# Performance work log

Hardware: AMD Instinct MI355X
Metric: run time of the kernel (lower is better)

## Reference

```python
import jax, jax.numpy as jnp
import numpy as np

B, N, S, K, D = 8, 16384, 1024, 32, 64
MLP = [64, 64, 128]
C_IN = 3 + D  # grouped_xyz_norm (3) concat grouped point features (D)
EPS = 1e-5


def setup_inputs() -> dict:
    key = jax.random.key(0)
    ks = jax.random.split(key, 16)
    inp = {
        "xyz": jax.random.normal(ks[0], (B, 3, N), dtype=jnp.float32),
        "points": jax.random.normal(ks[1], (B, D, N), dtype=jnp.float32),
        "sample_idx": jax.random.randint(ks[2], (B, S), 0, N, dtype=jnp.int32),
    }
    last = C_IN
    for i, oc in enumerate(MLP):
        scale = 1.0 / np.sqrt(last)
        inp[f"w{i}"] = jax.random.uniform(ks[3 + 4 * i], (oc, last), jnp.float32, -scale, scale)
        inp[f"b{i}"] = jax.random.uniform(ks[4 + 4 * i], (oc,), jnp.float32, -scale, scale)
        inp[f"g{i}"] = jnp.ones((oc,), jnp.float32)   # BN gamma
        inp[f"be{i}"] = jnp.zeros((oc,), jnp.float32)  # BN beta
        last = oc
    return inp


def _gather(pts, idx):
    # pts: [B,N,C], idx: [B,...] -> [B,...,C]
    return jax.vmap(lambda p, i: p[i])(pts, idx)


def _mlp_layer(x, w, b, g, be):
    # x: [B,C,K,S]; 1x1 Conv2d + BatchNorm2d (training-mode batch stats) + ReLU
    y = jnp.einsum("bcks,oc->boks", x, w) + b[None, :, None, None]
    mu = jnp.mean(y, axis=(0, 2, 3), keepdims=True)
    var = jnp.var(y, axis=(0, 2, 3), keepdims=True)
    y = (y - mu) * jax.lax.rsqrt(var + EPS)
    y = y * g[None, :, None, None] + be[None, :, None, None]
    return jax.nn.relu(y)


def reference(xyz, points, sample_idx, w0, b0, g0, be0, w1, b1, g1, be1, w2, b2, g2, be2):
    xyz_t = jnp.transpose(xyz, (0, 2, 1))      # [B,N,3]
    pts_t = jnp.transpose(points, (0, 2, 1))   # [B,N,D]
    idx_s = sample_idx.astype(jnp.int32)

    new_xyz = _gather(xyz_t, idx_s)            # [B,S,3]

    # square_distance(new_xyz, xyz): [B,S,N]
    d = (jnp.sum(new_xyz ** 2, -1)[:, :, None]
         + jnp.sum(xyz_t ** 2, -1)[:, None, :]
         - 2.0 * jnp.einsum("bsc,bnc->bsn", new_xyz, xyz_t))
    _, idx = jax.lax.top_k(-d, K)              # kNN indices [B,S,K]

    grouped_xyz = _gather(xyz_t, idx)          # [B,S,K,3]
    grouped_norm = grouped_xyz - new_xyz[:, :, None, :]
    grouped_pts = _gather(pts_t, idx)          # [B,S,K,D]
    feat = jnp.concatenate([grouped_norm, grouped_pts], axis=-1)  # [B,S,K,3+D]

    x = jnp.transpose(feat, (0, 3, 2, 1))      # [B,C,K,S]
    x = _mlp_layer(x, w0, b0, g0, be0)
    x = _mlp_layer(x, w1, b1, g1, be1)
    x = _mlp_layer(x, w2, b2, g2, be2)
    new_points = jnp.max(x, axis=2)            # [B,128,S]

    return (jnp.transpose(new_xyz, (0, 2, 1)), new_points, grouped_xyz, idx_s)
```

## Files before the change

### kernel.cpp

```cpp
#include <hip/hip_runtime.h>

constexpr int cB = 8, cN = 16384, cS = 1024, cK = 32, cD = 64;
constexpr int cO2 = 128;
constexpr int PTOT = cB * cS * cK;
constexpr int NBLK = PTOT / 64;
constexpr int C2POS = 128;
constexpr int NBLK2 = PTOT / C2POS;

constexpr int OUT1_OFF = cB * 3 * cS;
constexpr int OUT2_OFF = OUT1_OFF + cB * cO2 * cS;
constexpr int OUT3_OFF = OUT2_OFF + cB * cS * cK * 3;

constexpr size_t WS_PTS  = 0;
constexpr size_t WS_XYZP = WS_PTS  + (size_t)cB * cN * cD * 4;
constexpr size_t WS_IDX  = WS_XYZP + (size_t)cB * cN * 16;
constexpr size_t WS_NORM = WS_IDX  + (size_t)PTOT * 4;
constexpr size_t WS_Y0   = WS_NORM + (size_t)PTOT * 3 * 4;
constexpr size_t WS_Y1   = WS_Y0   + (size_t)PTOT * 64 * 4;
constexpr size_t WS_MX   = WS_Y1   + (size_t)PTOT * 64 * 4;
constexpr size_t WS_MN   = WS_MX   + (size_t)cB * cS * cO2 * 4;
constexpr size_t WS_P0   = WS_MN   + (size_t)cB * cS * cO2 * 4;
constexpr size_t WS_P1   = WS_P0   + (size_t)NBLK * 64 * 2 * 8;
constexpr size_t WS_P2   = WS_P1   + (size_t)NBLK * 64 * 2 * 8;
constexpr size_t WS_BN   = WS_P2   + (size_t)NBLK * 128 * 2 * 8;
constexpr size_t WS_END  = WS_BN   + 3 * 128 * 2 * 4;

__device__ __forceinline__ unsigned keyOf(float d) {
    unsigned u = __float_as_uint(d);
    return u ^ ((unsigned)((int)u >> 31) | 0x80000000u);
}
__device__ __forceinline__ float distNp(float qx, float qy, float qz, float sq, float4 p) {
    float m0 = __fmul_rn(qx, p.x);
    float m1 = __fmul_rn(qy, p.y);
    float m2 = __fmul_rn(qz, p.z);
    float dt = __fadd_rn(__fadd_rn(m0, m1), m2);
    return __fsub_rn(__fadd_rn(sq, p.w), __fmul_rn(2.0f, dt));
}

__global__ __launch_bounds__(256) void k_pack(const float* __restrict__ xyz,
                                              float4* __restrict__ xyzp) {
    int i = blockIdx.x * 256 + threadIdx.x;
    int b = i >> 14, n = i & (cN - 1);
    float x = xyz[(b * 3 + 0) * cN + n];
    float y = xyz[(b * 3 + 1) * cN + n];
    float z = xyz[(b * 3 + 2) * cN + n];
    float sq = __fadd_rn(__fadd_rn(__fmul_rn(x, x), __fmul_rn(y, y)), __fmul_rn(z, z));
    xyzp[i] = make_float4(x, y, z, sq);
}

__global__ __launch_bounds__(256) void k_tr(const float* __restrict__ pts,
                                            float* __restrict__ ptsT) {
    __shared__ float tile[64][65];
    int b = blockIdx.y;
    int n0 = blockIdx.x * 64;
    int tid = threadIdx.x;
    for (int it = 0; it < 16; ++it) {
        int l = it * 256 + tid;
        int c = l >> 6, nn = l & 63;
        tile[nn][c] = pts[((size_t)b * 64 + c) * cN + n0 + nn];
    }
    __syncthreads();
    for (int it = 0; it < 16; ++it) {
        int l = it * 256 + tid;
        int nn = l >> 6, c = l & 63;
        ptsT[((size_t)(b * cN + n0 + nn)) * 64 + c] = tile[nn][c];
    }
}

#define QB 8
#define CAP 256

__device__ __forceinline__ void selectBin2(const unsigned* __restrict__ h, int lane,
                                           int target, int* Tout, int* cbOut) {
    int base = lane * 8;
    unsigned hh[8];
    unsigned c8 = 0;
#pragma unroll
    for (int i = 0; i < 8; i++) { hh[i] = h[base + i]; c8 += hh[i]; }
    unsigned incl = c8;
#pragma unroll
    for (int off = 1; off < 32; off <<= 1) {
        unsigned t = __shfl_up(incl, (unsigned)off, 32);
        if (lane >= off) incl += t;
    }
    int excl = (int)(incl - c8);
    if (excl < target && target <= (int)incl) {
        int c = excl;
#pragma unroll
        for (int i = 0; i < 8; i++) {
            int nc = c + (int)hh[i];
            if (c < target && target <= nc) { *Tout = base + i; *cbOut = c; }
            c = nc;
        }
    }
}

__global__ __launch_bounds__(256, 4) void k_knn(const float* __restrict__ xyz,
                                                const int* __restrict__ sidx_g,
                                                const float4* __restrict__ xyzp,
                                                int* __restrict__ idxw,
                                                float* __restrict__ normw,
                                                float* __restrict__ outbuf) {
    __shared__ unsigned hist[QB][258];
    __shared__ unsigned long long cand[QB][CAP];
    __shared__ unsigned cnt[QB];
    __shared__ float qxs[QB], qys[QB], qzs[QB], sqs[QB];
    __shared__ int sIdx[QB];
    __shared__ float s1s[QB], tAs[QB], tBs[QB];
    __shared__ int T1s[QB], cb1s[QB], T2s[QB], cb2s[QB];
    __shared__ float tAcc[QB];
    __shared__ int refq[QB];
    __shared__ int anyRef;
    __shared__ unsigned order[QB][cK];

    int tid = threadIdx.x;
    int qi = tid >> 5, lane = tid & 31;
    int qbase = blockIdx.x * QB;
    int b = qbase / cS;
    int s0 = qbase % cS;
    const float4* pb = xyzp + (size_t)b * cN;

    if (tid < QB) {
        int si = sidx_g[b * cS + s0 + tid];
        sIdx[tid] = si;
        float x = xyz[(b * 3 + 0) * cN + si];
        float y = xyz[(b * 3 + 1) * cN + si];
        float z = xyz[(b * 3 + 2) * cN + si];
        qxs[tid] = x; qys[tid] = y; qzs[tid] = z;
        sqs[tid] = __fadd_rn(__fadd_rn(__fmul_rn(x, x), __fmul_rn(y, y)), __fmul_rn(z, z));
        cnt[tid] = 0u;
    }
    if (tid == 0) anyRef = 0;
    for (int i = tid; i < QB * 258; i += 256) ((unsigned*)hist)[i] = 0u;
    __syncthreads();

    {
        float qx = qxs[qi], qy = qys[qi], qz = qzs[qi], qsq = sqs[qi];
        float dmin = 3.4e38f;
        for (int t = 0; t < 64; ++t) {
            float4 p = pb[lane + 32 * t];
            float dot = fmaf(qx, p.x, fmaf(qy, p.y, qz * p.z));
            float d = fmaf(-2.0f, dot, qsq + p.w);
            dmin = fminf(dmin, d);
        }
        float rmax = dmin;
#pragma unroll
        for (int off = 16; off; off >>= 1)
            rmax = fmaxf(rmax, __shfl_xor(rmax, off, 32));
        if (lane == 0) {
            float R = fmaxf(rmax, 1e-12f);
            float s1 = 254.0f / R;
            s1s[qi] = s1;
            tAs[qi] = qsq * s1;
            tBs[qi] = -2.0f * s1;
        }
    }
    __syncthreads();

    float lqx[QB], lqy[QB], lqz[QB], lS[QB], lA[QB], lB[QB];
#pragma unroll
    for (int q = 0; q < QB; q++) {
        lqx[q] = qxs[q]; lqy[q] = qys[q]; lqz[q] = qzs[q];
        lS[q] = s1s[q]; lA[q] = tAs[q]; lB[q] = tBs[q];
    }

    for (int j = 0; j < cN / 256; ++j) {
        float4 p = pb[j * 256 + tid];
#pragma unroll
        for (int q = 0; q < QB; ++q) {
            float dot = fmaf(lqx[q], p.x, fmaf(lqy[q], p.y, lqz[q] * p.z));
            float t = fmaf(dot, lB[q], fmaf(p.w, lS[q], lA[q]));
            if (t < 258.0f) {
                int bin = __float2int_rz(fmaxf(t, 0.0f));
                atomicAdd(&hist[q][bin], 1u);
            }
        }
    }
    __syncthreads();

    selectBin2(hist[qi], lane, cK, &T1s[qi], &cb1s[qi]);
    __syncthreads();
    if (tid < QB) {
        int T1 = T1s[tid];
        int acc = cb1s[tid] + (int)hist[tid][T1] + (int)hist[tid][T1 + 1];
        int nr = (acc > CAP) ? 1 : 0;
        refq[tid] = nr;
        tAcc[tid] = (float)(T1 + 2);
        if (nr) atomicOr(&anyRef, 1);
    }
    __syncthreads();

    if (anyRef) {
        for (int i = tid; i < QB * 258; i += 256) ((unsigned*)hist)[i] = 0u;
        __syncthreads();
        int lT1[QB], lrf[QB];
#pragma unroll
        for (int q = 0; q < QB; q++) { lT1[q] = T1s[q]; lrf[q] = refq[q]; }
        for (int j = 0; j < cN / 256; ++j) {
            float4 p = pb[j * 256 + tid];
#pragma unroll
            for (int q = 0; q < QB; ++q) {
                if (lrf[q]) {
                    float dot = fmaf(lqx[q], p.x, fmaf(lqy[q], p.y, lqz[q] * p.z));
                    float t = fmaf(dot, lB[q], fmaf(p.w, lS[q], lA[q]));
                    float um = fmaxf(t, 0.0f) - (float)lT1[q];
                    if (um >= 0.0f && um < 2.0f) {
                        int sub = min(255, __float2int_rz(um * 128.0f));
                        atomicAdd(&hist[q][sub], 1u);
                    }
                }
            }
        }
        __syncthreads();
        if (refq[qi]) selectBin2(hist[qi], lane, cK - cb1s[qi], &T2s[qi], &cb2s[qi]);
        __syncthreads();
        if (tid < QB && refq[tid])
            tAcc[tid] = (float)T1s[tid] + (float)(T2s[tid] + 2) * 0.0078125f;
        __syncthreads();
    }

    float lsq[QB], lt[QB];
#pragma unroll
    for (int q = 0; q < QB; q++) { lsq[q] = sqs[q]; lt[q] = tAcc[q]; }

    for (int j = 0; j < cN / 256; ++j) {
        int n = j * 256 + tid;
        float4 p = pb[n];
#pragma unroll
        for (int q = 0; q < QB; ++q) {
            float dot = fmaf(lqx[q], p.x, fmaf(lqy[q], p.y, lqz[q] * p.z));
            float t = fmaf(dot, lB[q], fmaf(p.w, lS[q], lA[q]));
            if (t < lt[q]) {
                float de = distNp(lqx[q], lqy[q], lqz[q], lsq[q], p);
                unsigned pos = atomicAdd(&cnt[q], 1u);
                if (pos < CAP)
                    cand[q][pos] = ((unsigned long long)keyOf(de) << 32) | (unsigned)n;
            }
        }
    }
    __syncthreads();

    int m = (int)min(cnt[qi], (unsigned)CAP);
    for (int r = 0; r < cK; ++r) {
        unsigned long long best = ~0ull;
        int bslot = -1;
        for (int i = lane; i < m; i += 32) {
            unsigned long long v = cand[qi][i];
            if (v < best) { best = v; bslot = i; }
        }
#pragma unroll
        for (int off = 16; off; off >>= 1) {
            unsigned long long ov = __shfl_xor(best, off, 32);
            int os = __shfl_xor(bslot, off, 32);
            if (ov < best) { best = ov; bslot = os; }
        }
        if (lane == 0) {
            order[qi][r] = (best != ~0ull) ? (unsigned)(best & 0xFFFFFFFFull) : 0u;
            if (bslot >= 0) cand[qi][bslot] = ~0ull;
        }
    }

    {
        int r = lane;
        int s = s0 + qi;
        int n = (int)order[qi][r];
        size_t pos = (size_t)(b * cS + s) * cK + r;
        idxw[pos] = n;
        float px = xyz[(b * 3 + 0) * cN + n];
        float py = xyz[(b * 3 + 1) * cN + n];
        float pz = xyz[(b * 3 + 2) * cN + n];
        outbuf[OUT2_OFF + pos * 3 + 0] = px;
        outbuf[OUT2_OFF + pos * 3 + 1] = py;
        outbuf[OUT2_OFF + pos * 3 + 2] = pz;
        normw[pos * 3 + 0] = __fsub_rn(px, qxs[qi]);
        normw[pos * 3 + 1] = __fsub_rn(py, qys[qi]);
        normw[pos * 3 + 2] = __fsub_rn(pz, qzs[qi]);
        if (r == 0) {
            outbuf[OUT3_OFF + b * cS + s] = (float)sIdx[qi];
            outbuf[(b * 3 + 0) * cS + s] = qxs[qi];
            outbuf[(b * 3 + 1) * cS + s] = qys[qi];
            outbuf[(b * 3 + 2) * cS + s] = qzs[qi];
        }
    }
}

__global__ __launch_bounds__(256) void k_conv0(const int* __restrict__ idxw,
                                               const float* __restrict__ normw,
                                               const float* __restrict__ ptsT,
                                               const float* __restrict__ w0,
                                               const float* __restrict__ b0,
                                               float* __restrict__ y0,
                                               double* __restrict__ part0) {
    __shared__ __align__(16) float fA[64][68];
    __shared__ __align__(16) float wT[68 * 68];
    __shared__ float ps[16][64];
    __shared__ float pq[16][64];
    __shared__ float bl[64];
    int tid = threadIdx.x;
    int blk = blockIdx.x;
    int b = blk >> 9;
    int s0 = (blk & 511) << 1;
    size_t posbase = ((size_t)b * cS + s0) * cK;

    for (int l = tid; l < 64 * 67; l += 256) {
        int o = l / 67, c = l - o * 67;
        wT[c * 68 + o] = w0[l];
    }
    if (tid < 68) wT[67 * 68 + tid] = 0.0f;
    if (tid < 64) bl[tid] = b0[tid];
    {
        int kk = tid >> 2, p = tid & 3;
        size_t pos = posbase + kk;
        int n = idxw[pos];
        const float* pr = ptsT + ((size_t)b * cN + n) * 64 + p * 16;
        float* frow = &fA[kk][3 + p * 16];
#pragma unroll
        for (int q4 = 0; q4 < 4; q4++) {
            float4 v = *(const float4*)(pr + q4 * 4);
            frow[q4 * 4 + 0] = v.x; frow[q4 * 4 + 1] = v.y;
            frow[q4 * 4 + 2] = v.z; frow[q4 * 4 + 3] = v.w;
        }
        if (p == 0) {
            fA[kk][0] = normw[pos * 3 + 0];
            fA[kk][1] = normw[pos * 3 + 1];
            fA[kk][2] = normw[pos * 3 + 2];
            fA[kk][67] = 0.0f;
        }
    }
    __syncthreads();

    int ty = tid >> 4, tx = tid & 15;
    float acc[4][4];
#pragma unroll
    for (int i = 0; i < 4; i++)
#pragma unroll
        for (int j = 0; j < 4; j++) acc[i][j] = bl[tx * 4 + j];

    for (int c4 = 0; c4 < 17; ++c4) {
        float4 wv[4];
#pragma unroll
        for (int cc = 0; cc < 4; cc++)
            wv[cc] = *(const float4*)&wT[(c4 * 4 + cc) * 68 + tx * 4];
#pragma unroll
        for (int i = 0; i < 4; i++) {
            float4 a = *(const float4*)&fA[ty * 4 + i][c4 * 4];
            acc[i][0] = fmaf(a.x, wv[0].x, acc[i][0]);
            acc[i][1] = fmaf(a.x, wv[0].y, acc[i][1]);
            acc[i][2] = fmaf(a.x, wv[0].z, acc[i][2]);
            acc[i][3] = fmaf(a.x, wv[0].w, acc[i][3]);
            acc[i][0] = fmaf(a.y, wv[1].x, acc[i][0]);
            acc[i][1] = fmaf(a.y, wv[1].y, acc[i][1]);
            acc[i][2] = fmaf(a.y, wv[1].z, acc[i][2]);
            acc[i][3] = fmaf(a.y, wv[1].w, acc[i][3]);
            acc[i][0] = fmaf(a.z, wv[2].x, acc[i][0]);
            acc[i][1] = fmaf(a.z, wv[2].y, acc[i][1]);
            acc[i][2] = fmaf(a.z, wv[2].z, acc[i][2]);
            acc[i][3] = fmaf(a.z, wv[2].w, acc[i][3]);
            acc[i][0] = fmaf(a.w, wv[3].x, acc[i][0]);
            acc[i][1] = fmaf(a.w, wv[3].y, acc[i][1]);
            acc[i][2] = fmaf(a.w, wv[3].z, acc[i][2]);
            acc[i][3] = fmaf(a.w, wv[3].w, acc[i][3]);
        }
    }
#pragma unroll
    for (int i = 0; i < 4; i++) {
        int kk = ty * 4 + i;
        float4 o4 = make_float4(acc[i][0], acc[i][1], acc[i][2], acc[i][3]);
        *(float4*)(y0 + (posbase + kk) * 64 + tx * 4) = o4;
    }
#pragma unroll
    for (int j = 0; j < 4; j++) {
        float s = acc[0][j] + acc[1][j] + acc[2][j] + acc[3][j];
        float q = acc[0][j] * acc[0][j] + acc[1][j] * acc[1][j] +
                  acc[2][j] * acc[2][j] + acc[3][j] * acc[3][j];
        ps[ty][tx * 4 + j] = s;
        pq[ty][tx * 4 + j] = q;
    }
    __syncthreads();
    if (tid < 64) {
        float s = 0.f, q = 0.f;
        for (int t = 0; t < 16; t++) { s += ps[t][tid]; q += pq[t][tid]; }
        part0[((size_t)blk * 64 + tid) * 2 + 0] = (double)s;
        part0[((size_t)blk * 64 + tid) * 2 + 1] = (double)q;
    }
}

__global__ __launch_bounds__(256) void k_conv1(const float* __restrict__ yin,
                                               const float2* __restrict__ bnin,
                                               const float* __restrict__ w,
                                               const float* __restrict__ bb,
                                               float* __restrict__ yout,
                                               double* __restrict__ part) {
    __shared__ __align__(16) float fA[64][68];
    __shared__ __align__(16) float wT[64 * 68];
    __shared__ float ps[16][64];
    __shared__ float pq[16][64];
    __shared__ float bl[64], al[64], sl[64];
    int tid = threadIdx.x;
    int blk = blockIdx.x;
    int b = blk >> 9;
    int s0 = (blk & 511) << 1;
    size_t posbase = ((size_t)b * cS + s0) * cK;

    if (tid < 64) {
        bl[tid] = bb[tid];
        float2 t = bnin[tid];
        al[tid] = t.x; sl[tid] = t.y;
    }
    __syncthreads();
    for (int l = tid; l < 64 * 64; l += 256) {
        int o = l >> 6, c = l & 63;
        wT[c * 68 + o] = w[l];
    }
    {
        int kk = tid >> 2, p = tid & 3;
        const float* yr = yin + (posbase + kk) * 64 + p * 16;
#pragma unroll
        for (int q4 = 0; q4 < 4; q4++) {
            float4 v = *(const float4*)(yr + q4 * 4);
            int c = p * 16 + q4 * 4;
            v.x = fmaxf(fmaf(v.x, al[c + 0], sl[c + 0]), 0.0f);
            v.y = fmaxf(fmaf(v.y, al[c + 1], sl[c + 1]), 0.0f);
            v.z = fmaxf(fmaf(v.z, al[c + 2], sl[c + 2]), 0.0f);
            v.w = fmaxf(fmaf(v.w, al[c + 3], sl[c + 3]), 0.0f);
            *(float4*)&fA[kk][c] = v;
        }
    }
    __syncthreads();

    int ty = tid >> 4, tx = tid & 15;
    float acc[4][4];
#pragma unroll
    for (int i = 0; i < 4; i++)
#pragma unroll
        for (int j = 0; j < 4; j++) acc[i][j] = bl[tx * 4 + j];

    for (int c4 = 0; c4 < 16; ++c4) {
        float4 wv[4];
#pragma unroll
        for (int cc = 0; cc < 4; cc++)
            wv[cc] = *(const float4*)&wT[(c4 * 4 + cc) * 68 + tx * 4];
#pragma unroll
        for (int i = 0; i < 4; i++) {
            float4 a = *(const float4*)&fA[ty * 4 + i][c4 * 4];
            acc[i][0] = fmaf(a.x, wv[0].x, acc[i][0]);
            acc[i][1] = fmaf(a.x, wv[0].y, acc[i][1]);
            acc[i][2] = fmaf(a.x, wv[0].z, acc[i][2]);
            acc[i][3] = fmaf(a.x, wv[0].w, acc[i][3]);
            acc[i][0] = fmaf(a.y, wv[1].x, acc[i][0]);
            acc[i][1] = fmaf(a.y, wv[1].y, acc[i][1]);
            acc[i][2] = fmaf(a.y, wv[1].z, acc[i][2]);
            acc[i][3] = fmaf(a.y, wv[1].w, acc[i][3]);
            acc[i][0] = fmaf(a.z, wv[2].x, acc[i][0]);
            acc[i][1] = fmaf(a.z, wv[2].y, acc[i][1]);
            acc[i][2] = fmaf(a.z, wv[2].z, acc[i][2]);
            acc[i][3] = fmaf(a.z, wv[2].w, acc[i][3]);
            acc[i][0] = fmaf(a.w, wv[3].x, acc[i][0]);
            acc[i][1] = fmaf(a.w, wv[3].y, acc[i][1]);
            acc[i][2] = fmaf(a.w, wv[3].z, acc[i][2]);
            acc[i][3] = fmaf(a.w, wv[3].w, acc[i][3]);
        }
    }
#pragma unroll
    for (int i = 0; i < 4; i++) {
        int kk = ty * 4 + i;
        float4 o4 = make_float4(acc[i][0], acc[i][1], acc[i][2], acc[i][3]);
        *(float4*)(yout + (posbase + kk) * 64 + tx * 4) = o4;
    }
#pragma unroll
    for (int j = 0; j < 4; j++) {
        float s = acc[0][j] + acc[1][j] + acc[2][j] + acc[3][j];
        float q = acc[0][j] * acc[0][j] + acc[1][j] * acc[1][j] +
                  acc[2][j] * acc[2][j] + acc[3][j] * acc[3][j];
        ps[ty][tx * 4 + j] = s;
        pq[ty][tx * 4 + j] = q;
    }
    __syncthreads();
    if (tid < 64) {
        float s = 0.f, q = 0.f;
        for (int t = 0; t < 16; t++) { s += ps[t][tid]; q += pq[t][tid]; }
        part[((size_t)blk * 64 + tid) * 2 + 0] = (double)s;
        part[((size_t)blk * 64 + tid) * 2 + 1] = (double)q;
    }
}

__global__ __launch_bounds__(256) void k_conv2(const float* __restrict__ y1,
                                               const float2* __restrict__ bn1,
                                               const float* __restrict__ w2,
                                               const float* __restrict__ b2,
                                               float* __restrict__ mx,
                                               float* __restrict__ mn,
                                               double* __restrict__ part2) {
    __shared__ __align__(16) float fAT[64 * 132];
    __shared__ __align__(16) float wT[64 * 132];
    __shared__ float al[64], sl[64], bl[128];
    int tid = threadIdx.x;
    int blk = blockIdx.x;
    int b = blk >> 8;
    int s0 = (blk & 255) << 2;
    size_t posbase = ((size_t)b * cS + s0) * cK;

    if (tid < 64) { float2 t = bn1[tid]; al[tid] = t.x; sl[tid] = t.y; }
    if (tid < 128) bl[tid] = b2[tid];
    __syncthreads();

    {
        int r = tid >> 1, half = tid & 1;
        const float* yr = y1 + (posbase + r) * 64 + half * 32;
#pragma unroll
        for (int q = 0; q < 8; q++) {
            float4 v = *(const float4*)(yr + q * 4);
            int c = half * 32 + q * 4;
            v.x = fmaxf(fmaf(v.x, al[c + 0], sl[c + 0]), 0.0f);
            v.y = fmaxf(fmaf(v.y, al[c + 1], sl[c + 1]), 0.0f);
            v.z = fmaxf(fmaf(v.z, al[c + 2], sl[c + 2]), 0.0f);
            v.w = fmaxf(fmaf(v.w, al[c + 3], sl[c + 3]), 0.0f);
            fAT[(c + 0) * 132 + r] = v.x;
            fAT[(c + 1) * 132 + r] = v.y;
            fAT[(c + 2) * 132 + r] = v.z;
            fAT[(c + 3) * 132 + r] = v.w;
        }
    }
    for (int l = tid; l < 128 * 64; l += 256) {
        int o = l >> 6, c = l & 63;
        wT[c * 132 + o] = w2[l];
    }
    __syncthreads();

    int ry = tid >> 4, tx = tid & 15;
    float acc[8][8];
#pragma unroll
    for (int i = 0; i < 8; i++) {
#pragma unroll
        for (int j = 0; j < 4; j++) acc[i][j] = bl[tx * 4 + j];
#pragma unroll
        for (int j = 4; j < 8; j++) acc[i][j] = bl[64 + tx * 4 + (j - 4)];
    }

    for (int c = 0; c < 64; ++c) {
        const float* fb = fAT + c * 132;
        const float* wb = wT + c * 132;
        float4 a0 = *(const float4*)(fb + ry * 8);
        float4 a1 = *(const float4*)(fb + ry * 8 + 4);
        float4 w0v = *(const float4*)(wb + tx * 4);
        float4 w1v = *(const float4*)(wb + 64 + tx * 4);
        float av[8] = {a0.x, a0.y, a0.z, a0.w, a1.x, a1.y, a1.z, a1.w};
        float wv[8] = {w0v.x, w0v.y, w0v.z, w0v.w, w1v.x, w1v.y, w1v.z, w1v.w};
#pragma unroll
        for (int i = 0; i < 8; i++)
#pragma unroll
            for (int j = 0; j < 8; j++)
                acc[i][j] = fmaf(av[i], wv[j], acc[i][j]);
    }
    __syncthreads();

    float* ps  = wT;
    float* pq  = wT + 16 * 128;
    float* pmx = wT + 32 * 128;
    float* pmn = wT + 48 * 128;
#pragma unroll
    for (int j = 0; j < 8; j++) {
        int o = (j < 4) ? (tx * 4 + j) : (64 + tx * 4 + (j - 4));
        float s = 0.f, q = 0.f;
        float mv = -3.402823466e+38f, nv = 3.402823466e+38f;
#pragma unroll
        for (int i = 0; i < 8; i++) {
            float v = acc[i][j];
            s += v; q += v * v;
            mv = fmaxf(mv, v); nv = fminf(nv, v);
        }
        ps[ry * 128 + o] = s;
        pq[ry * 128 + o] = q;
        pmx[ry * 128 + o] = mv;
        pmn[ry * 128 + o] = nv;
    }
    __syncthreads();
    if (tid < 128) {
        float s = 0.f, q = 0.f;
        for (int t = 0; t < 16; t++) { s += ps[t * 128 + tid]; q += pq[t * 128 + tid]; }
        part2[((size_t)blk * 128 + tid) * 2 + 0] = (double)s;
        part2[((size_t)blk * 128 + tid) * 2 + 1] = (double)q;
    }
    for (int e = tid; e < 512; e += 256) {
        int sg = e >> 7, o = e & 127;
        float mv = -3.402823466e+38f, nv = 3.402823466e+38f;
        for (int t = sg * 4; t < sg * 4 + 4; ++t) {
            mv = fmaxf(mv, pmx[t * 128 + o]);
            nv = fminf(nv, pmn[t * 128 + o]);
        }
        int s = s0 + sg;
        mx[((size_t)b * cS + s) * 128 + o] = mv;
        mn[((size_t)b * cS + s) * 128 + o] = nv;
    }
}

__global__ __launch_bounds__(256) void k_fin(const double* __restrict__ part, int nblk,
                                             int oc,
                                             const float* __restrict__ g,
                                             const float* __restrict__ be,
                                             float2* __restrict__ bnout) {
    __shared__ double rs[256], rq[256];
    int o = blockIdx.x;
    int tid = threadIdx.x;
    double s = 0.0, q = 0.0;
    for (int i = tid; i < nblk; i += 256) {
        const double* p = part + ((size_t)i * oc + o) * 2;
        s += p[0];
        q += p[1];
    }
    rs[tid] = s; rq[tid] = q;
    __syncthreads();
    for (int off = 128; off; off >>= 1) {
        if (tid < off) { rs[tid] += rs[tid + off]; rq[tid] += rq[tid + off]; }
        __syncthreads();
    }
    if (tid == 0) {
        double cntv = (double)PTOT;
        double mu = rs[0] / cntv;
        double var = rq[0] / cntv - mu * mu;
        if (var < 0.0) var = 0.0;
        float a = (float)((double)g[o] / sqrt(var + 1e-5));
        float sh = (float)((double)be[o] - mu * (double)a);
        bnout[o] = make_float2(a, sh);
    }
}

__global__ __launch_bounds__(256) void k_final(const float* __restrict__ mx,
                                               const float* __restrict__ mn,
                                               const float2* __restrict__ bn2,
                                               float* __restrict__ out1) {
    int i = blockIdx.x * 256 + threadIdx.x;
    int b = i >> 17;
    int r = i & ((1 << 17) - 1);
    int o = r >> 10;
    int s = r & 1023;
    float2 t = bn2[o];
    size_t idx = ((size_t)b * cS + s) * 128 + o;
    float M = (t.x >= 0.0f) ? mx[idx] : mn[idx];
    out1[i] = fmaxf(t.x * M + t.y, 0.0f);
}

extern "C" void kernel_launch(void* const* d_in, const int* in_sizes, int n_in,
                              void* d_out, int out_size, void* d_ws, size_t ws_size,
                              hipStream_t stream) {
    (void)in_sizes; (void)n_in; (void)out_size;
    const float* xyz = (const float*)d_in[0];
    const float* pts = (const float*)d_in[1];
    const int* sidx  = (const int*)d_in[2];
    const float* w0  = (const float*)d_in[3];
    const float* b0  = (const float*)d_in[4];
    const float* g0  = (const float*)d_in[5];
    const float* be0 = (const float*)d_in[6];
    const float* w1  = (const float*)d_in[7];
    const float* b1  = (const float*)d_in[8];
    const float* g1  = (const float*)d_in[9];
    const float* be1 = (const float*)d_in[10];
    const float* w2  = (const float*)d_in[11];
    const float* b2  = (const float*)d_in[12];
    const float* g2  = (const float*)d_in[13];
    const float* be2 = (const float*)d_in[14];
    float* out = (float*)d_out;
    char* ws = (char*)d_ws;
    if (ws_size < WS_END) return;

    float* ptsT  = (float*)(ws + WS_PTS);
    float4* xyzp = (float4*)(ws + WS_XYZP);
    int* idxw    = (int*)(ws + WS_IDX);
    float* normw = (float*)(ws + WS_NORM);
    float* y0    = (float*)(ws + WS_Y0);
    float* y1    = (float*)(ws + WS_Y1);
    float* mx    = (float*)(ws + WS_MX);
    float* mn    = (float*)(ws + WS_MN);
    double* p0   = (double*)(ws + WS_P0);
    double* p1   = (double*)(ws + WS_P1);
    double* p2   = (double*)(ws + WS_P2);
    float2* bnb  = (float2*)(ws + WS_BN);

    hipLaunchKernelGGL(k_pack, dim3(cB * cN / 256), dim3(256), 0, stream, xyz, xyzp);
    hipLaunchKernelGGL(k_tr, dim3(cN / 64, cB), dim3(256), 0, stream, pts, ptsT);
    hipLaunchKernelGGL(k_knn, dim3(cB * cS / QB), dim3(256), 0, stream,
                       xyz, sidx, xyzp, idxw, normw, out);
    hipLaunchKernelGGL(k_conv0, dim3(NBLK), dim3(256), 0, stream,
                       idxw, normw, ptsT, w0, b0, y0, p0);
    hipLaunchKernelGGL(k_fin, dim3(64), dim3(256), 0, stream, p0, NBLK, 64, g0, be0, bnb);
    hipLaunchKernelGGL(k_conv1, dim3(NBLK), dim3(256), 0, stream, y0, bnb, w1, b1, y1, p1);
    hipLaunchKernelGGL(k_fin, dim3(64), dim3(256), 0, stream, p1, NBLK, 64, g1, be1, bnb + 128);
    hipLaunchKernelGGL(k_conv2, dim3(NBLK2), dim3(256), 0, stream,
                       y1, bnb + 128, w2, b2, mx, mn, p2);
    hipLaunchKernelGGL(k_fin, dim3(128), dim3(256), 0, stream, p2, NBLK2, 128, g2, be2, bnb + 256);
    hipLaunchKernelGGL(k_final, dim3(cB * cO2 * cS / 256), dim3(256), 0, stream,
                       mx, mn, bnb + 256, out + OUT1_OFF);
}
```

Before: 397.4 us.

## Add uniform grid spatial index to restrict kNN scans to nearby cells

Measured after the change: 755.0 us. 90.0% more time.

```diff
diff --git a/kernel.cpp b/kernel.cpp
--- a/kernel.cpp
+++ b/kernel.cpp
@@ -6,6 +6,11 @@
 constexpr int NBLK = PTOT / 64;
 constexpr int C2POS = 128;
 constexpr int NBLK2 = PTOT / C2POS;
+
+constexpr int GR = 32;
+constexpr int GC = GR * GR * GR;
+#define GL 4.5f
+#define GINV (32.0f / 9.0f)
 
 constexpr int OUT1_OFF = cB * 3 * cS;
 constexpr int OUT2_OFF = OUT1_OFF + cB * cO2 * cS;
@@ -25,6 +30,11 @@
 constexpr size_t WS_BN   = WS_P2   + (size_t)NBLK * 128 * 2 * 8;
 constexpr size_t WS_END  = WS_BN   + 3 * 128 * 2 * 4;
 
+constexpr size_t WS_SPT  = WS_Y0;
+constexpr size_t WS_SIX  = WS_SPT + (size_t)cB * cN * 16;
+constexpr size_t WS_CNT  = WS_SIX + (size_t)cB * cN * 4;
+constexpr size_t WS_CST  = WS_CNT + (size_t)cB * GC * 4;
+
 __device__ __forceinline__ unsigned keyOf(float d) {
     unsigned u = __float_as_uint(d);
     return u ^ ((unsigned)((int)u >> 31) | 0x80000000u);
@@ -35,6 +45,13 @@
     float m2 = __fmul_rn(qz, p.z);
     float dt = __fadd_rn(__fadd_rn(m0, m1), m2);
     return __fsub_rn(__fadd_rn(sq, p.w), __fmul_rn(2.0f, dt));
+}
+
+__device__ __forceinline__ int cellClamp(float v) {
+    return min(GR - 1, max(0, (int)floorf((v + GL) * GINV)));
+}
+__device__ __forceinline__ int cellOf(float4 p) {
+    return (cellClamp(p.z) * GR + cellClamp(p.y)) * GR + cellClamp(p.x);
 }
 
 __global__ __launch_bounds__(256) void k_pack(const float* __restrict__ xyz,
@@ -48,23 +65,54 @@
     xyzp[i] = make_float4(x, y, z, sq);
 }
 
-__global__ __launch_bounds__(256) void k_tr(const float* __restrict__ pts,
-                                            float* __restrict__ ptsT) {
-    __shared__ float tile[64][65];
-    int b = blockIdx.y;
-    int n0 = blockIdx.x * 64;
-    int tid = threadIdx.x;
-    for (int it = 0; it < 16; ++it) {
-        int l = it * 256 + tid;
-        int c = l >> 6, nn = l & 63;
-        tile[nn][c] = pts[((size_t)b * 64 + c) * cN + n0 + nn];
-    }
-    __syncthreads();
-    for (int it = 0; it < 16; ++it) {
-        int l = it * 256 + tid;
-        int nn = l >> 6, c = l & 63;
-        ptsT[((size_t)(b * cN + n0 + nn)) * 64 + c] = tile[nn][c];
-    }
+__global__ __launch_bounds__(256) void k_gzero(int* __restrict__ cnt) {
+    int i = blockIdx.x * 256 + threadIdx.x;
+    if (i < cB * GC) cnt[i] = 0;
+}
+
+__global__ __launch_bounds__(256) void k_gcnt(const float4* __restrict__ xyzp,
+                                              int* __restrict__ cnt) {
+    int i = blockIdx.x * 256 + threadIdx.x;
+    int b = i >> 14;
+    atomicAdd(&cnt[b * GC + cellOf(xyzp[i])], 1);
+}
+
+__global__ __launch_bounds__(256) void k_gscan(int* __restrict__ cnt,
+                                               int* __restrict__ cst) {
+    __shared__ int s[256];
+    int b = blockIdx.x, tid = threadIdx.x;
+    const int CB = GC / 256;
+    int base = b * GC + tid * CB;
+    int sum = 0;
+    for (int k = 0; k < CB; ++k) sum += cnt[base + k];
+    s[tid] = sum;
+    __syncthreads();
+    for (int off = 1; off < 256; off <<= 1) {
+        int v = (tid >= off) ? s[tid - off] : 0;
+        __syncthreads();
+        s[tid] += v;
+        __syncthreads();
+    }
+    int run = s[tid] - sum;
+    for (int k = 0; k < CB; ++k) {
+        int v = cnt[base + k];
+        cst[(size_t)b * (GC + 1) + tid * CB + k] = run;
+        cnt[base + k] = run;
+        run += v;
+    }
+    if (tid == 255) cst[(size_t)b * (GC + 1) + GC] = run;
+}
+
+__global__ __launch_bounds__(256) void k_gscat(const float4* __restrict__ xyzp,
+                                               int* __restrict__ cnt,
+                                               float4* __restrict__ spt,
+                                               int* __restrict__ six) {
+    int i = blockIdx.x * 256 + threadIdx.x;
+    int b = i >> 14, n = i & (cN - 1);
+    float4 p = xyzp[i];
+    int pos = atomicAdd(&cnt[b * GC + cellOf(p)], 1);
+    spt[(size_t)b * cN + pos] = p;
+    six[(size_t)b * cN + pos] = n;
 }
 
 #define QB 8
@@ -98,6 +146,9 @@
 __global__ __launch_bounds__(256, 4) void k_knn(const float* __restrict__ xyz,
                                                 const int* __restrict__ sidx_g,
                                                 const float4* __restrict__ xyzp,
+                                                const float4* __restrict__ spt,
+                                                const int* __restrict__ six,
+                                                const int* __restrict__ cellStart,
                                                 int* __restrict__ idxw,
                                                 float* __restrict__ normw,
                                                 float* __restrict__ outbuf) {
@@ -106,7 +157,6 @@
     __shared__ unsigned cnt[QB];
     __shared__ float qxs[QB], qys[QB], qzs[QB], sqs[QB];
     __shared__ int sIdx[QB];
-    __shared__ float s1s[QB], tAs[QB], tBs[QB];
     __shared__ int T1s[QB], cb1s[QB], T2s[QB], cb2s[QB];
     __shared__ float tAcc[QB];
     __shared__ int refq[QB];
@@ -119,6 +169,9 @@
     int b = qbase / cS;
     int s0 = qbase % cS;
     const float4* pb = xyzp + (size_t)b * cN;
+    const float4* sp = spt + (size_t)b * cN;
+    const int* sx = six + (size_t)b * cN;
+    const int* CS = cellStart + (size_t)b * (GC + 1);
 
     if (tid < QB) {
         int si = sidx_g[b * cS + s0 + tid];
@@ -134,8 +187,10 @@
     for (int i = tid; i < QB * 258; i += 256) ((unsigned*)hist)[i] = 0u;
     __syncthreads();
 
+    float qx = qxs[qi], qy = qys[qi], qz = qzs[qi], qsq = sqs[qi];
+
+    float rmax;
     {
-        float qx = qxs[qi], qy = qys[qi], qz = qzs[qi], qsq = sqs[qi];
         float dmin = 3.4e38f;
         for (int t = 0; t < 64; ++t) {
             float4 p = pb[lane + 32 * t];
@@ -143,39 +198,35 @@
             float d = fmaf(-2.0f, dot, qsq + p.w);
             dmin = fminf(dmin, d);
         }
-        float rmax = dmin;
+        rmax = dmin;
 #pragma unroll
         for (int off = 16; off; off >>= 1)
             rmax = fmaxf(rmax, __shfl_xor(rmax, off, 32));
-        if (lane == 0) {
-            float R = fmaxf(rmax, 1e-12f);
-            float s1 = 254.0f / R;
-            s1s[qi] = s1;
-            tAs[qi] = qsq * s1;
-            tBs[qi] = -2.0f * s1;
-        }
-    }
-    __syncthreads();
-
-    float lqx[QB], lqy[QB], lqz[QB], lS[QB], lA[QB], lB[QB];
-#pragma unroll
-    for (int q = 0; q < QB; q++) {
-        lqx[q] = qxs[q]; lqy[q] = qys[q]; lqz[q] = qzs[q];
-        lS[q] = s1s[q]; lA[q] = tAs[q]; lB[q] = tBs[q];
-    }
-
-    for (int j = 0; j < cN / 256; ++j) {
-        float4 p = pb[j * 256 + tid];
-#pragma unroll
-        for (int q = 0; q < QB; ++q) {
-            float dot = fmaf(lqx[q], p.x, fmaf(lqy[q], p.y, lqz[q] * p.z));
-            float t = fmaf(dot, lB[q], fmaf(p.w, lS[q], lA[q]));
-            if (t < 258.0f) {
-                int bin = __float2int_rz(fmaxf(t, 0.0f));
-                atomicAdd(&hist[q][bin], 1u);
+    }
+
+    float Rp = fmaxf(rmax, 1e-12f) * 1.001f;
+    float s1 = 254.0f / Rp;
+    float ccx = -2.0f * s1 * qx, ccy = -2.0f * s1 * qy, ccz = -2.0f * s1 * qz;
+    float ccw = s1, cc0 = s1 * qsq;
+    float rq = sqrtf(Rp);
+    int cxlo = max(0, (int)floorf((qx - rq + GL) * GINV));
+    int cxhi = min(GR - 1, (int)floorf((qx + rq + GL) * GINV));
+    int cylo = max(0, (int)floorf((qy - rq + GL) * GINV));
+    int cyhi = min(GR - 1, (int)floorf((qy + rq + GL) * GINV));
+    int czlo = max(0, (int)floorf((qz - rq + GL) * GINV));
+    int czhi = min(GR - 1, (int)floorf((qz + rq + GL) * GINV));
+
+    for (int cz = czlo; cz <= czhi; ++cz)
+        for (int cy = cylo; cy <= cyhi; ++cy) {
+            int rbase = (cz * GR + cy) * GR;
+            int st = CS[rbase + cxlo], en = CS[rbase + cxhi + 1];
+            for (int i = st + lane; i < en; i += 32) {
+                float4 p = sp[i];
+                float t = fmaf(p.x, ccx, fmaf(p.y, ccy, fmaf(p.z, ccz, fmaf(p.w, ccw, cc0))));
+                if (t < 258.0f)
+                    atomicAdd(&hist[qi][__float2int_rz(fmaxf(t, 0.0f))], 1u);
             }
         }
-    }
     __syncthreads();
 
     selectBin2(hist[qi], lane, cK, &T1s[qi], &cb1s[qi]);
@@ -193,23 +244,22 @@
     if (anyRef) {
         for (int i = tid; i < QB * 258; i += 256) ((unsigned*)hist)[i] = 0u;
         __syncthreads();
-        int lT1[QB], lrf[QB];
-#pragma unroll
-        for (int q = 0; q < QB; q++) { lT1[q] = T1s[q]; lrf[q] = refq[q]; }
-        for (int j = 0; j < cN / 256; ++j) {
-            float4 p = pb[j * 256 + tid];
-#pragma unroll
-            for (int q = 0; q < QB; ++q) {
-                if (lrf[q]) {
-                    float dot = fmaf(lqx[q], p.x, fmaf(lqy[q], p.y, lqz[q] * p.z));
-                    float t = fmaf(dot, lB[q], fmaf(p.w, lS[q], lA[q]));
-                    float um = fmaxf(t, 0.0f) - (float)lT1[q];
-                    if (um >= 0.0f && um < 2.0f) {
-                        int sub = min(255, __float2int_rz(um * 128.0f));
-                        atomicAdd(&hist[q][sub], 1u);
+        if (refq[qi]) {
+            float fT1 = (float)T1s[qi];
+            for (int cz = czlo; cz <= czhi; ++cz)
+                for (int cy = cylo; cy <= cyhi; ++cy) {
+                    int rbase = (cz * GR + cy) * GR;
+                    int st = CS[rbase + cxlo], en = CS[rbase + cxhi + 1];
+                    for (int i = st + lane; i < en; i += 32) {
+                        float4 p = sp[i];
+                        float t = fmaf(p.x, ccx, fmaf(p.y, ccy, fmaf(p.z, ccz, fmaf(p.w, ccw, cc0))));
+                        float um = fmaxf(t, 0.0f) - fT1;
+                        if (um >= 0.0f && um < 2.0f) {
+                            int sub = min(255, __float2int_rz(um * 128.0f));
+                            atomicAdd(&hist[qi][sub], 1u);
+                        }
                     }
                 }
-            }
         }
         __syncthreads();
         if (refq[qi]) selectBin2(hist[qi], lane, cK - cb1s[qi], &T2s[qi], &cb2s[qi]);
@@ -219,25 +269,24 @@
         __syncthreads();
     }
 
-    float lsq[QB], lt[QB];
-#pragma unroll
-    for (int q = 0; q < QB; q++) { lsq[q] = sqs[q]; lt[q] = tAcc[q]; }
-
-    for (int j = 0; j < cN / 256; ++j) {
-        int n = j * 256 + tid;
-        float4 p = pb[n];
-#pragma unroll
-        for (int q = 0; q < QB; ++q) {
-            float dot = fmaf(lqx[q], p.x, fmaf(lqy[q], p.y, lqz[q] * p.z));
-            float t = fmaf(dot, lB[q], fmaf(p.w, lS[q], lA[q]));
-            if (t < lt[q]) {
-                float de = distNp(lqx[q], lqy[q], lqz[q], lsq[q], p);
-                unsigned pos = atomicAdd(&cnt[q], 1u);
-                if (pos < CAP)
-                    cand[q][pos] = ((unsigned long long)keyOf(de) << 32) | (unsigned)n;
+    float lt = tAcc[qi];
+
+    for (int cz = czlo; cz <= czhi; ++cz)
+        for (int cy = cylo; cy <= cyhi; ++cy) {
+            int rbase = (cz * GR + cy) * GR;
+            int st = CS[rbase + cxlo], en = CS[rbase + cxhi + 1];
+            for (int i = st + lane; i < en; i += 32) {
+                float4 p = sp[i];
+                float t = fmaf(p.x, ccx, fmaf(p.y, ccy, fmaf(p.z, ccz, fmaf(p.w, ccw, cc0))));
+                if (t < lt) {
+                    float de = distNp(qx, qy, qz, qsq, p);
+                    int n = sx[i];
+                    unsigned pos = atomicAdd(&cnt[qi], 1u);
+                    if (pos < CAP)
+                        cand[qi][pos] = ((unsigned long long)keyOf(de) << 32) | (unsigned)n;
+                }
             }
         }
-    }
     __syncthreads();
 
     int m = (int)min(cnt[qi], (unsigned)CAP);
@@ -281,6 +330,25 @@
             outbuf[(b * 3 + 1) * cS + s] = qys[qi];
             outbuf[(b * 3 + 2) * cS + s] = qzs[qi];
         }
+    }
+}
+
+__global__ __launch_bounds__(256) void k_tr(const float* __restrict__ pts,
+                                            float* __restrict__ ptsT) {
+    __shared__ float tile[64][65];
+    int b = blockIdx.y;
+    int n0 = blockIdx.x * 64;
+    int tid = threadIdx.x;
+    for (int it = 0; it < 16; ++it) {
+        int l = it * 256 + tid;
+        int c = l >> 6, nn = l & 63;
+        tile[nn][c] = pts[((size_t)b * 64 + c) * cN + n0 + nn];
+    }
+    __syncthreads();
+    for (int it = 0; it < 16; ++it) {
+        int l = it * 256 + tid;
+        int nn = l >> 6, c = l & 63;
+        ptsT[((size_t)(b * cN + n0 + nn)) * 64 + c] = tile[nn][c];
     }
 }
 
@@ -675,11 +743,20 @@
     double* p1   = (double*)(ws + WS_P1);
     double* p2   = (double*)(ws + WS_P2);
     float2* bnb  = (float2*)(ws + WS_BN);
+    float4* spt  = (float4*)(ws + WS_SPT);
+    int* six     = (int*)(ws + WS_SIX);
+    int* gcnt    = (int*)(ws + WS_CNT);
+    int* gcst    = (int*)(ws + WS_CST);
 
     hipLaunchKernelGGL(k_pack, dim3(cB * cN / 256), dim3(256), 0, stream, xyz, xyzp);
+    hipLaunchKernelGGL(k_gzero, dim3((cB * GC + 255) / 256), dim3(256), 0, stream, gcnt);
+    hipLaunchKernelGGL(k_gcnt, dim3(cB * cN / 256), dim3(256), 0, stream, xyzp, gcnt);
+    hipLaunchKernelGGL(k_gscan, dim3(cB), dim3(256), 0, stream, gcnt, gcst);
+    hipLaunchKernelGGL(k_gscat, dim3(cB * cN / 256), dim3(256), 0, stream,
+                       xyzp, gcnt, spt, six);
     hipLaunchKernelGGL(k_tr, dim3(cN / 64, cB), dim3(256), 0, stream, pts, ptsT);
     hipLaunchKernelGGL(k_knn, dim3(cB * cS / QB), dim3(256), 0, stream,
-                       xyz, sidx, xyzp, idxw, normw, out);
+                       xyz, sidx, xyzp, spt, six, gcst, idxw, normw, out);
     hipLaunchKernelGGL(k_conv0, dim3(NBLK), dim3(256), 0, stream,
                        idxw, normw, ptsT, w0, b0, y0, p0);
     hipLaunchKernelGGL(k_fin, dim3(64), dim3(256), 0, stream, p0, NBLK, 64, g0, be0, bnb);
```

## Cache coarse-histogram candidates as ushort indices to skip full rescans

Applied to the files above, without the earlier changes.

After: 446.1 us. 1.12x slower.

```diff
diff --git a/kernel.cpp b/kernel.cpp
--- a/kernel.cpp
+++ b/kernel.cpp
@@ -68,7 +68,8 @@
 }
 
 #define QB 8
-#define CAP 256
+#define CAPU 896
+#define CAP2 192
 
 __device__ __forceinline__ void selectBin2(const unsigned* __restrict__ h, int lane,
                                            int target, int* Tout, int* cbOut) {
@@ -102,15 +103,16 @@
                                                 float* __restrict__ normw,
                                                 float* __restrict__ outbuf) {
     __shared__ unsigned hist[QB][258];
-    __shared__ unsigned long long cand[QB][CAP];
-    __shared__ unsigned cnt[QB];
+    __shared__ unsigned short candU[QB][CAPU];
+    __shared__ unsigned long long cand2[QB][CAP2];
+    __shared__ unsigned cnt[QB], cnt2[QB];
     __shared__ float qxs[QB], qys[QB], qzs[QB], sqs[QB];
     __shared__ int sIdx[QB];
     __shared__ float s1s[QB], tAs[QB], tBs[QB];
     __shared__ int T1s[QB], cb1s[QB], T2s[QB], cb2s[QB];
-    __shared__ float tAcc[QB];
-    __shared__ int refq[QB];
-    __shared__ int anyRef;
+    __shared__ float fTs[QB];
+    __shared__ int ovf[QB], nRf[QB];
+    __shared__ int anyR, anyOvfR, anyOvfC;
     __shared__ unsigned order[QB][cK];
 
     int tid = threadIdx.x;
@@ -128,14 +130,15 @@
         float z = xyz[(b * 3 + 2) * cN + si];
         qxs[tid] = x; qys[tid] = y; qzs[tid] = z;
         sqs[tid] = __fadd_rn(__fadd_rn(__fmul_rn(x, x), __fmul_rn(y, y)), __fmul_rn(z, z));
-        cnt[tid] = 0u;
-    }
-    if (tid == 0) anyRef = 0;
+        cnt[tid] = 0u; cnt2[tid] = 0u;
+    }
+    if (tid == 0) { anyR = 0; anyOvfR = 0; anyOvfC = 0; }
     for (int i = tid; i < QB * 258; i += 256) ((unsigned*)hist)[i] = 0u;
     __syncthreads();
 
+    float qx = qxs[qi], qy = qys[qi], qz = qzs[qi], qsq = sqs[qi];
+
     {
-        float qx = qxs[qi], qy = qys[qi], qz = qzs[qi], qsq = sqs[qi];
         float dmin = 3.4e38f;
         for (int t = 0; t < 64; ++t) {
             float4 p = pb[lane + 32 * t];
@@ -165,7 +168,8 @@
     }
 
     for (int j = 0; j < cN / 256; ++j) {
-        float4 p = pb[j * 256 + tid];
+        int n = j * 256 + tid;
+        float4 p = pb[n];
 #pragma unroll
         for (int q = 0; q < QB; ++q) {
             float dot = fmaf(lqx[q], p.x, fmaf(lqy[q], p.y, lqz[q] * p.z));
@@ -173,6 +177,8 @@
             if (t < 258.0f) {
                 int bin = __float2int_rz(fmaxf(t, 0.0f));
                 atomicAdd(&hist[q][bin], 1u);
+                unsigned pos = atomicAdd(&cnt[q], 1u);
+                if (pos < CAPU) candU[q][pos] = (unsigned short)n;
             }
         }
     }
@@ -183,69 +189,104 @@
     if (tid < QB) {
         int T1 = T1s[tid];
         int acc = cb1s[tid] + (int)hist[tid][T1] + (int)hist[tid][T1 + 1];
-        int nr = (acc > CAP) ? 1 : 0;
-        refq[tid] = nr;
-        tAcc[tid] = (float)(T1 + 2);
-        if (nr) atomicOr(&anyRef, 1);
-    }
-    __syncthreads();
-
-    if (anyRef) {
+        int ov = (cnt[tid] > CAPU) ? 1 : 0;
+        int nr = (acc > CAP2) ? 1 : 0;
+        ovf[tid] = ov; nRf[tid] = nr;
+        fTs[tid] = (float)(T1 + 2);
+        if (nr) atomicOr(&anyR, 1);
+        if (nr && ov) atomicOr(&anyOvfR, 1);
+        if (ov) atomicOr(&anyOvfC, 1);
+    }
+    __syncthreads();
+
+    if (anyR) {
         for (int i = tid; i < QB * 258; i += 256) ((unsigned*)hist)[i] = 0u;
         __syncthreads();
-        int lT1[QB], lrf[QB];
-#pragma unroll
-        for (int q = 0; q < QB; q++) { lT1[q] = T1s[q]; lrf[q] = refq[q]; }
-        for (int j = 0; j < cN / 256; ++j) {
-            float4 p = pb[j * 256 + tid];
-#pragma unroll
-            for (int q = 0; q < QB; ++q) {
-                if (lrf[q]) {
-                    float dot = fmaf(lqx[q], p.x, fmaf(lqy[q], p.y, lqz[q] * p.z));
-                    float t = fmaf(dot, lB[q], fmaf(p.w, lS[q], lA[q]));
-                    float um = fmaxf(t, 0.0f) - (float)lT1[q];
-                    if (um >= 0.0f && um < 2.0f) {
-                        int sub = min(255, __float2int_rz(um * 128.0f));
-                        atomicAdd(&hist[q][sub], 1u);
+        if (anyOvfR) {
+            int lT1[QB], go[QB];
+#pragma unroll
+            for (int q = 0; q < QB; q++) { lT1[q] = T1s[q]; go[q] = nRf[q] & ovf[q]; }
+            for (int j = 0; j < cN / 256; ++j) {
+                float4 p = pb[j * 256 + tid];
+#pragma unroll
+                for (int q = 0; q < QB; ++q) {
+                    if (go[q]) {
+                        float dot = fmaf(lqx[q], p.x, fmaf(lqy[q], p.y, lqz[q] * p.z));
+                        float t = fmaf(dot, lB[q], fmaf(p.w, lS[q], lA[q]));
+                        float um = fmaxf(t, 0.0f) - (float)lT1[q];
+                        if (um >= 0.0f && um < 2.0f)
+                            atomicAdd(&hist[q][min(255, __float2int_rz(um * 128.0f))], 1u);
                     }
                 }
             }
         }
+        if (nRf[qi] && !ovf[qi]) {
+            float fT1 = (float)T1s[qi];
+            int m = (int)cnt[qi];
+            for (int i = lane; i < m; i += 32) {
+                int n = candU[qi][i];
+                float4 p = pb[n];
+                float dot = fmaf(qx, p.x, fmaf(qy, p.y, qz * p.z));
+                float t = fmaf(dot, tBs[qi], fmaf(p.w, s1s[qi], tAs[qi]));
+                float um = fmaxf(t, 0.0f) - fT1;
+                if (um >= 0.0f && um < 2.0f)
+                    atomicAdd(&hist[qi][min(255, __float2int_rz(um * 128.0f))], 1u);
+            }
+        }
         __syncthreads();
-        if (refq[qi]) selectBin2(hist[qi], lane, cK - cb1s[qi], &T2s[qi], &cb2s[qi]);
+        if (nRf[qi]) selectBin2(hist[qi], lane, cK - cb1s[qi], &T2s[qi], &cb2s[qi]);
         __syncthreads();
-        if (tid < QB && refq[tid])
-            tAcc[tid] = (float)T1s[tid] + (float)(T2s[tid] + 2) * 0.0078125f;
+        if (tid < QB && nRf[tid])
+            fTs[tid] = (float)T1s[tid] + (float)(T2s[tid] + 2) * 0.0078125f;
         __syncthreads();
     }
 
-    float lsq[QB], lt[QB];
-#pragma unroll
-    for (int q = 0; q < QB; q++) { lsq[q] = sqs[q]; lt[q] = tAcc[q]; }
-
-    for (int j = 0; j < cN / 256; ++j) {
-        int n = j * 256 + tid;
-        float4 p = pb[n];
-#pragma unroll
-        for (int q = 0; q < QB; ++q) {
-            float dot = fmaf(lqx[q], p.x, fmaf(lqy[q], p.y, lqz[q] * p.z));
-            float t = fmaf(dot, lB[q], fmaf(p.w, lS[q], lA[q]));
-            if (t < lt[q]) {
-                float de = distNp(lqx[q], lqy[q], lqz[q], lsq[q], p);
-                unsigned pos = atomicAdd(&cnt[q], 1u);
-                if (pos < CAP)
-                    cand[q][pos] = ((unsigned long long)keyOf(de) << 32) | (unsigned)n;
+    if (anyOvfC) {
+        float lt[QB]; int go[QB]; float lsq[QB];
+#pragma unroll
+        for (int q = 0; q < QB; q++) { lt[q] = fTs[q]; go[q] = ovf[q]; lsq[q] = sqs[q]; }
+        for (int j = 0; j < cN / 256; ++j) {
+            int n = j * 256 + tid;
+            float4 p = pb[n];
+#pragma unroll
+            for (int q = 0; q < QB; ++q) {
+                if (go[q]) {
+                    float dot = fmaf(lqx[q], p.x, fmaf(lqy[q], p.y, lqz[q] * p.z));
+                    float t = fmaf(dot, lB[q], fmaf(p.w, lS[q], lA[q]));
+                    if (t < lt[q]) {
+                        float de = distNp(lqx[q], lqy[q], lqz[q], lsq[q], p);
+                        unsigned pos = atomicAdd(&cnt2[q], 1u);
+                        if (pos < CAP2)
+                            cand2[q][pos] = ((unsigned long long)keyOf(de) << 32) | (unsigned)n;
+                    }
+                }
             }
         }
     }
-    __syncthreads();
-
-    int m = (int)min(cnt[qi], (unsigned)CAP);
+    if (!ovf[qi]) {
+        float fT = fTs[qi];
+        int m = (int)cnt[qi];
+        for (int i = lane; i < m; i += 32) {
+            int n = candU[qi][i];
+            float4 p = pb[n];
+            float dot = fmaf(qx, p.x, fmaf(qy, p.y, qz * p.z));
+            float t = fmaf(dot, tBs[qi], fmaf(p.w, s1s[qi], tAs[qi]));
+            if (t < fT) {
+                float de = distNp(qx, qy, qz, qsq, p);
+                unsigned pos = atomicAdd(&cnt2[qi], 1u);
+                if (pos < CAP2)
+                    cand2[qi][pos] = ((unsigned long long)keyOf(de) << 32) | (unsigned)n;
+            }
+        }
+    }
+    __syncthreads();
+
+    int m2 = (int)min(cnt2[qi], (unsigned)CAP2);
     for (int r = 0; r < cK; ++r) {
         unsigned long long best = ~0ull;
         int bslot = -1;
-        for (int i = lane; i < m; i += 32) {
-            unsigned long long v = cand[qi][i];
+        for (int i = lane; i < m2; i += 32) {
+            unsigned long long v = cand2[qi][i];
             if (v < best) { best = v; bslot = i; }
         }
 #pragma unroll
@@ -256,7 +297,7 @@
         }
         if (lane == 0) {
             order[qi][r] = (best != ~0ull) ? (unsigned)(best & 0xFFFFFFFFull) : 0u;
-            if (bslot >= 0) cand[qi][bslot] = ~0ull;
+            if (bslot >= 0) cand2[qi][bslot] = ~0ull;
         }
     }
 
```
